# Optimization experiments

Hardware: AMD Instinct MI355X
Metric: run time of the kernel (lower is better)

Reference implementation:

```python
import jax, jax.numpy as jnp
import numpy as np

TAG_SIZE = 32
START = 30
STOP = 31
NEG = -10000.0
V, D, H, T = 100000, 256, 512, 4096  # vocab, embed_dim, hidden_dim, seq_len
HD = H // 2  # per-direction hidden


def setup_inputs() -> dict:
    key = jax.random.key(0)
    ks = jax.random.split(key, 12)
    s = 1.0 / np.sqrt(HD)

    def lstm_params(k):
        k1, k2, k3, k4 = jax.random.split(k, 4)
        return (jax.random.uniform(k1, (4 * HD, D), minval=-s, maxval=s),
                jax.random.uniform(k2, (4 * HD, HD), minval=-s, maxval=s),
                jax.random.uniform(k3, (4 * HD,), minval=-s, maxval=s),
                jax.random.uniform(k4, (4 * HD,), minval=-s, maxval=s))

    Wih_f, Whh_f, bih_f, bhh_f = lstm_params(ks[0])
    Wih_b, Whh_b, bih_b, bhh_b = lstm_params(ks[1])
    seq = jax.random.randint(ks[2], (T,), 0, V)
    E = jax.random.normal(ks[3], (V, D)) * 0.02
    h0 = jax.random.normal(ks[4], (2, HD))  # torch.randn initial hidden (fwd, bwd)
    c0 = jax.random.normal(ks[5], (2, HD))
    W_out = jax.random.normal(ks[6], (TAG_SIZE, H)) * 0.02
    b_out = jnp.zeros((TAG_SIZE,))
    transitions = jax.random.normal(ks[7], (TAG_SIZE, TAG_SIZE))
    transitions = transitions.at[START, :].set(NEG).at[:, STOP].set(NEG)
    return dict(seq=seq, E=E,
                Wih_f=Wih_f, Whh_f=Whh_f, bih_f=bih_f, bhh_f=bhh_f,
                Wih_b=Wih_b, Whh_b=Whh_b, bih_b=bih_b, bhh_b=bhh_b,
                h0=h0, c0=c0, W_out=W_out, b_out=b_out, transitions=transitions)


def _lstm_dir(x, h0, c0, Wih, Whh, bih, bhh):
    # x: (T, D). Precompute input projections for all steps at once.
    xg = x @ Wih.T + (bih + bhh)  # (T, 4*HD)

    def step(carry, xt):
        h, c = carry
        g = xt + h @ Whh.T
        i, f, gg, o = jnp.split(g, 4)  # torch gate order: i, f, g, o
        i = jax.nn.sigmoid(i); f = jax.nn.sigmoid(f)
        gg = jnp.tanh(gg); o = jax.nn.sigmoid(o)
        c = f * c + i * gg
        h = o * jnp.tanh(c)
        return (h, c), h

    _, hs = jax.lax.scan(step, (h0, c0), xg)
    return hs  # (T, HD)


def reference(seq, E, Wih_f, Whh_f, bih_f, bhh_f, Wih_b, Whh_b, bih_b, bhh_b,
              h0, c0, W_out, b_out, transitions):
    x = E[seq]  # (T, D)
    hf = _lstm_dir(x, h0[0], c0[0], Wih_f, Whh_f, bih_f, bhh_f)
    hb = _lstm_dir(x[::-1], h0[1], c0[1], Wih_b, Whh_b, bih_b, bhh_b)[::-1]
    feats = jnp.concatenate([hf, hb], axis=-1) @ W_out.T + b_out  # (T, TAG)

    # Viterbi: fused per-step (TAG x TAG) max-plus update in one scan.
    init = jnp.full((TAG_SIZE,), NEG).at[START].set(0.0)

    def vstep(fv, feat):
        scores = fv[None, :] + transitions  # [next_tag, prev_tag]
        bp = jnp.argmax(scores, axis=1)     # backpointers (emission is constant per next_tag)
        fv = jnp.max(scores, axis=1) + feat
        return fv, bp

    fv, bps = jax.lax.scan(vstep, init, feats)
    terminal = fv + transitions[STOP]
    best = jnp.argmax(terminal)
    score = terminal[best]

    def btstep(b, bp):
        nb = bp[b]
        return nb, nb

    _, path_rev = jax.lax.scan(btstep, best, bps[::-1])
    # drop the step into <START>, reverse, append terminal best tag -> length T
    path = jnp.concatenate([path_rev[::-1][1:], best[None]])
    return score, path
```

## Files before the change

### kernel.cpp

```cpp
#include <hip/hip_runtime.h>
#include <hip/hip_bf16.h>
#include <stdint.h>

#define T_LEN 4096
#define D_DIM 256
#define HDIM 256
#define G4 1024
#define NTAGS 32
#define START_TAG 30
#define STOP_TAG 31

typedef unsigned long long u64;
typedef unsigned int u32;

__device__ __forceinline__ float sigf(float x){ return 1.0f/(1.0f+expf(-x)); }

__global__ __launch_bounds__(256) void k_xg(const int* __restrict__ seq,
    const float* __restrict__ E,
    const float* __restrict__ Wf, const float* __restrict__ bihf, const float* __restrict__ bhhf,
    const float* __restrict__ Wb, const float* __restrict__ bihb, const float* __restrict__ bhhb,
    float* __restrict__ xg_f, float* __restrict__ xg_b)
{
    __shared__ __align__(16) float xsh[8][D_DIM];
    __shared__ int sq[8];
    const int b = blockIdx.x, tb = b >> 3, cb = b & 7, j = threadIdx.x;
    if (j < 8) sq[j] = seq[tb*8 + j];
    __syncthreads();
    #pragma unroll
    for (int r = 0; r < 8; ++r) xsh[r][j] = E[(size_t)sq[r]*D_DIM + j];
    __syncthreads();
    const int col = cb*256 + j;
    const int d   = col >> 10;
    const int row = col & 1023;
    const float* W = d ? Wb : Wf;
    const float bias = d ? (bihb[row] + bhhb[row]) : (bihf[row] + bhhf[row]);
    const float4* wr = reinterpret_cast<const float4*>(W + (size_t)row*D_DIM);
    float acc[8];
    #pragma unroll
    for (int r=0;r<8;++r) acc[r] = 0.f;
    for (int kk = 0; kk < D_DIM/4; ++kk){
        float4 wv = wr[kk];
        #pragma unroll
        for (int r=0;r<8;++r){
            float4 xv = reinterpret_cast<const float4*>(xsh[r])[kk];
            acc[r] = fmaf(wv.x, xv.x, fmaf(wv.y, xv.y, fmaf(wv.z, xv.z, fmaf(wv.w, xv.w, acc[r]))));
        }
    }
    #pragma unroll
    for (int r=0;r<8;++r){
        const int t = tb*8 + r;
        const float v = acc[r] + bias;
        if (d == 0) xg_f[(size_t)t*G4 + row] = v;
        else        xg_b[(size_t)(T_LEN-1-t)*G4 + row] = v;
    }
}

__global__ __launch_bounds__(256,1) void k_lstm(
    const float* __restrict__ Whh_f, const float* __restrict__ Whh_b,
    const float* __restrict__ xgf, const float* __restrict__ xgb,
    const float* __restrict__ h0, const float* __restrict__ c0,
    float* __restrict__ hs_f, float* __restrict__ hs_b,
    u64* __restrict__ hbuf_all)
{
    const int blk = blockIdx.x;
    const int d   = blk >> 5;
    const int sb  = blk & 31;
    const int ulo = sb * 8;
    const int j = threadIdx.x;
    const int r = j & 31;
    const int o = j >> 5;
    const int g_r = r >> 3;
    const int u_r = r & 7;
    const int row_global = g_r*256 + ulo + u_r;

    const float* __restrict__ Whh = d ? Whh_b : Whh_f;
    const float* __restrict__ xg  = d ? xgb : xgf;
    float* __restrict__ hs = d ? hs_b : hs_f;
    u64* __restrict__ hb = hbuf_all + (size_t)d*2*HDIM;

    __shared__ __align__(16) char wbuf[32*1024];
    __shared__ float h_sh[HDIM];
    __shared__ float partial[2*256];

    {
        const float4* src = reinterpret_cast<const float4*>(Whh + (size_t)row_global*HDIM + o*32);
        #pragma unroll
        for (int i = 0; i < 8; ++i){
            *reinterpret_cast<float4*>(wbuf + ((r*1024 + (o*8+i)*16) ^ ((r&7)<<4))) = src[i];
        }
    }
    h_sh[j] = h0[d*HDIM + j];
    float c = (j < 8) ? c0[d*HDIM + ulo + j] : 0.0f;
    float xgc = xg[row_global];
    __syncthreads();

    for (int t = 0; t < T_LEN; ++t){
        if (t > 0){
            const u32 want = (u32)t;
            u64* p = &hb[(size_t)(t&1)*HDIM + j];
            u64 pk = __hip_atomic_load(p, __ATOMIC_RELAXED, __HIP_MEMORY_SCOPE_AGENT);
            while ((u32)(pk >> 32) != want){
                pk = __hip_atomic_load(p, __ATOMIC_RELAXED, __HIP_MEMORY_SCOPE_AGENT);
            }
            h_sh[j] = __uint_as_float((u32)pk);
            asm volatile("s_waitcnt lgkmcnt(0)" ::: "memory");
        }
        float acc = 0.0f;
        {
            const float4* hvp = reinterpret_cast<const float4*>(h_sh + o*32);
            #pragma unroll
            for (int i = 0; i < 8; ++i){
                float4 wv = *reinterpret_cast<const float4*>(wbuf + ((r*1024 + (o*8+i)*16) ^ ((r&7)<<4)));
                float4 hv = hvp[i];
                acc = fmaf(wv.x, hv.x, fmaf(wv.y, hv.y, fmaf(wv.z, hv.z, fmaf(wv.w, hv.w, acc))));
            }
        }
        partial[(t&1)*256 + o*32 + r] = acc;
        __syncthreads();
        if (j < 32){
            const int par = t & 1;
            float s = xgc;
            #pragma unroll
            for (int oo = 0; oo < 8; ++oo) s += partial[par*256 + oo*32 + j];
            const float val = (g_r == 2) ? tanhf(s) : sigf(s);
            const float fv_ = __shfl(val,  8 + u_r, 64);
            const float gv_ = __shfl(val, 16 + u_r, 64);
            const float ov_ = __shfl(val, 24 + u_r, 64);
            if (j < 8){
                c = fv_*c + val*gv_;
                const float h = ov_*tanhf(c);
                const int ug = ulo + j;
                const u64 pk = ((u64)(u32)(t+1) << 32) | (u64)__float_as_uint(h);
                __hip_atomic_store(&hb[(size_t)((t+1)&1)*HDIM + ug], pk,
                                   __ATOMIC_RELAXED, __HIP_MEMORY_SCOPE_AGENT);
                hs[(size_t)(d==0 ? t : (T_LEN-1-t))*HDIM + ug] = h;
            }
            if (t+1 < T_LEN) xgc = xg[(size_t)(t+1)*G4 + row_global];
        }
    }
}

__global__ __launch_bounds__(256) void k_feats(
    const float* __restrict__ hs_f, const float* __restrict__ hs_b,
    const float* __restrict__ W_out, const float* __restrict__ b_out,
    float* __restrict__ feats)
{
    __shared__ __align__(16) float fsh[8][512];
    const int tb = blockIdx.x, j = threadIdx.x;
    #pragma unroll
    for (int r=0;r<8;++r){
        const int t = tb*8 + r;
        fsh[r][j]       = hs_f[(size_t)t*HDIM + j];
        fsh[r][256 + j] = hs_b[(size_t)t*HDIM + j];
    }
    __syncthreads();
    const int tsub = j >> 5, tag = j & 31;
    const float4* wr = reinterpret_cast<const float4*>(W_out + (size_t)tag*512);
    float acc = b_out[tag];
    for (int kk=0; kk<128; ++kk){
        float4 wvv = wr[kk];
        float4 hv = reinterpret_cast<const float4*>(fsh[tsub])[kk];
        acc = fmaf(wvv.x, hv.x, fmaf(wvv.y, hv.y, fmaf(wvv.z, hv.z, fmaf(wvv.w, hv.w, acc))));
    }
    feats[(size_t)(tb*8+tsub)*NTAGS + tag] = acc;
}

__global__ __launch_bounds__(256,1) void k_viterbi(
    const float* __restrict__ feats, const float* __restrict__ trans,
    unsigned char* __restrict__ bp_g, float* __restrict__ out)
{
    __shared__ __align__(16) float fbuf[2][256*NTAGS];
    __shared__ float fv_sh[NTAGS];
    __shared__ float term_sh[NTAGS];
    __shared__ int best_sh;
    const int j = threadIdx.x;
    const int n = j & 31, ph = (j >> 5) & 1;
    const bool scanlane = (j < 64);
    float tr[16];
    if (scanlane){
        #pragma unroll
        for (int i=0;i<16;++i) tr[i] = trans[n*NTAGS + ph*16 + i];
    }
    float fv = (n == START_TAG) ? 0.0f : -10000.0f;

    const int CH = 256, NCH = T_LEN / CH;
    for (int idx = j; idx < CH*NTAGS; idx += 256) fbuf[0][idx] = feats[idx];
    __syncthreads();
    for (int cc = 0; cc < NCH; ++cc){
        const int buf = cc & 1;
        if (scanlane){
            for (int s = 0; s < CH; ++s){
                const int t = cc*CH + s;
                const float f = fbuf[buf][s*NTAGS + n];
                if (ph == 0) fv_sh[n] = fv;
                float bestv = -1e30f; int bestp = 0;
                #pragma unroll
                for (int i=0;i<16;++i){
                    const int p = ph*16 + i;
                    const float v = fv_sh[p] + tr[i];
                    if (v > bestv){ bestv = v; bestp = p; }
                }
                const float ov = __shfl_xor(bestv, 32, 64);
                const int   op = __shfl_xor(bestp, 32, 64);
                const float lowv  = ph ? ov    : bestv;
                const int   lowp  = ph ? op    : bestp;
                const float highv = ph ? bestv : ov;
                const int   highp = ph ? bestp : op;
                float wvv = lowv; int wp = lowp;
                if (highv > lowv){ wvv = highv; wp = highp; }
                if (ph == 0) bp_g[(size_t)t*NTAGS + n] = (unsigned char)wp;
                fv = wvv + f;
            }
        } else if (cc + 1 < NCH){
            const int nb = (cc+1) & 1;
            const float* src = feats + (size_t)(cc+1)*CH*NTAGS;
            for (int idx = j - 64; idx < CH*NTAGS; idx += 192) fbuf[nb][idx] = src[idx];
        }
        __syncthreads();
    }

    if (scanlane && ph == 0) term_sh[n] = fv + trans[STOP_TAG*NTAGS + n];
    __syncthreads();
    if (j == 0){
        float bv = term_sh[0]; int bi = 0;
        for (int p = 1; p < NTAGS; ++p){
            if (term_sh[p] > bv){ bv = term_sh[p]; bi = p; }
        }
        out[0] = bv;
        out[1 + (T_LEN-1)] = (float)bi;
        best_sh = bi;
    }
    __syncthreads();
    unsigned char* bp_sh = reinterpret_cast<unsigned char*>(fbuf);
    int b = best_sh;
    for (int cc2 = 3; cc2 >= 0; --cc2){
        const u32* src = reinterpret_cast<const u32*>(bp_g + (size_t)cc2*1024*NTAGS);
        u32* dst = reinterpret_cast<u32*>(bp_sh);
        for (int idx = j; idx < 8192; idx += 256) dst[idx] = src[idx];
        __syncthreads();
        if (j == 0){
            for (int tt = 1023; tt >= 0; --tt){
                const int t = cc2*1024 + tt;
                if (t == 0) break;
                const int nb2 = bp_sh[tt*NTAGS + b];
                out[1 + (t-1)] = (float)nb2;
                b = nb2;
            }
        }
        __syncthreads();
    }
}

extern "C" void kernel_launch(void* const* d_in, const int* in_sizes, int n_in,
                              void* d_out, int out_size, void* d_ws, size_t ws_size,
                              hipStream_t stream)
{
    const int*   seq   = (const int*)  d_in[0];
    const float* E     = (const float*)d_in[1];
    const float* Wih_f = (const float*)d_in[2];
    const float* Whh_f = (const float*)d_in[3];
    const float* bih_f = (const float*)d_in[4];
    const float* bhh_f = (const float*)d_in[5];
    const float* Wih_b = (const float*)d_in[6];
    const float* Whh_b = (const float*)d_in[7];
    const float* bih_b = (const float*)d_in[8];
    const float* bhh_b = (const float*)d_in[9];
    const float* h0    = (const float*)d_in[10];
    const float* c0    = (const float*)d_in[11];
    const float* W_out = (const float*)d_in[12];
    const float* b_out = (const float*)d_in[13];
    const float* trans = (const float*)d_in[14];

    char* ws = (char*)d_ws;
    float* xg_f  = (float*)(ws);
    float* xg_b  = (float*)(ws + (size_t)(16u<<20));
    float* hs_f  = (float*)(ws + (size_t)(32u<<20));
    float* hs_b  = (float*)(ws + (size_t)(36u<<20));
    float* feats = (float*)(ws + (size_t)(40u<<20));
    unsigned char* bp = (unsigned char*)(ws + (size_t)(40u<<20) + (512u<<10));
    u64* hbuf    = (u64*)(ws + (size_t)(40u<<20) + (640u<<10));

    k_xg<<<dim3(4096), dim3(256), 0, stream>>>(seq, E, Wih_f, bih_f, bhh_f,
                                               Wih_b, bih_b, bhh_b, xg_f, xg_b);
    k_lstm<<<dim3(64), dim3(256), 0, stream>>>(Whh_f, Whh_b, xg_f, xg_b, h0, c0, hs_f, hs_b, hbuf);
    k_feats<<<dim3(512), dim3(256), 0, stream>>>(hs_f, hs_b, W_out, b_out, feats);
    k_viterbi<<<dim3(1), dim3(256), 0, stream>>>(feats, trans, bp, (float*)d_out);
}
```

Baseline: 6.950 ms.

## Shrink LSTM recurrence to 8 blocks per direction with 128KB LDS weights

The persistent LSTM kernel now runs 8 workgroups per direction instead of 32. Each workgroup owns 32 hidden units (128 gate rows, 128KB of Whh in LDS), and each row is split across two lanes that are reduced with a shuffle rather than a shared-memory partial-sum pass. Locally produced h values are written straight into a double-buffered shared array, so only the other 224 units are polled from global memory each step. The aim is fewer participants in the cross-block spin synchronisation and less intra-block reduction latency per timestep. The cost is more serial FMA work per thread (128 FMAs) and very large LDS use per block.

```diff
diff --git a/kernel.cpp b/kernel.cpp
--- a/kernel.cpp
+++ b/kernel.cpp
@@ -63,80 +63,87 @@
     u64* __restrict__ hbuf_all)
 {
     const int blk = blockIdx.x;
-    const int d   = blk >> 5;
-    const int sb  = blk & 31;
-    const int ulo = sb * 8;
+    const int d   = blk >> 3;
+    const int sb  = blk & 7;
+    const int ulo = sb * 32;
     const int j = threadIdx.x;
-    const int r = j & 31;
-    const int o = j >> 5;
-    const int g_r = r >> 3;
-    const int u_r = r & 7;
-    const int row_global = g_r*256 + ulo + u_r;
+    const int w = j >> 6;
+    const int l = j & 63;
+    const int half = l & 1;
+    const int rb   = w*32 + (l >> 1);
+    const int g_r  = rb & 3;
+    const int u_loc= rb >> 2;
+    const int row_global = g_r*256 + ulo + u_loc;
+    const bool prod = ((l & 7) == 0);
+    const int ug = ulo + w*8 + (l >> 3);
 
     const float* __restrict__ Whh = d ? Whh_b : Whh_f;
     const float* __restrict__ xg  = d ? xgb : xgf;
     float* __restrict__ hs = d ? hs_b : hs_f;
     u64* __restrict__ hb = hbuf_all + (size_t)d*2*HDIM;
 
-    __shared__ __align__(16) char wbuf[32*1024];
-    __shared__ float h_sh[HDIM];
-    __shared__ float partial[2*256];
+    __shared__ __align__(16) char wbuf[128*1024];
+    __shared__ float h_sh[2][HDIM];
 
     {
-        const float4* src = reinterpret_cast<const float4*>(Whh + (size_t)row_global*HDIM + o*32);
+        const float4* src = reinterpret_cast<const float4*>(Whh + (size_t)row_global*HDIM + half*128);
         #pragma unroll
-        for (int i = 0; i < 8; ++i){
-            *reinterpret_cast<float4*>(wbuf + ((r*1024 + (o*8+i)*16) ^ ((r&7)<<4))) = src[i];
-        }
-    }
-    h_sh[j] = h0[d*HDIM + j];
-    float c = (j < 8) ? c0[d*HDIM + ulo + j] : 0.0f;
-    float xgc = xg[row_global];
+        for (int i = 0; i < 32; ++i){
+            const int byte = (rb*1024 + half*512 + i*16) ^ ((rb&7)<<4);
+            *reinterpret_cast<float4*>(wbuf + byte) = src[i];
+        }
+    }
+    h_sh[0][j] = h0[d*HDIM + j];
+    float c = 0.0f;
+    if (prod) c = c0[d*HDIM + ug];
+    float xgc = (half == 0) ? xg[row_global] : 0.0f;
     __syncthreads();
 
     for (int t = 0; t < T_LEN; ++t){
+        const int par = t & 1;
         if (t > 0){
-            const u32 want = (u32)t;
-            u64* p = &hb[(size_t)(t&1)*HDIM + j];
-            u64 pk = __hip_atomic_load(p, __ATOMIC_RELAXED, __HIP_MEMORY_SCOPE_AGENT);
-            while ((u32)(pk >> 32) != want){
-                pk = __hip_atomic_load(p, __ATOMIC_RELAXED, __HIP_MEMORY_SCOPE_AGENT);
-            }
-            h_sh[j] = __uint_as_float((u32)pk);
-            asm volatile("s_waitcnt lgkmcnt(0)" ::: "memory");
-        }
+            const bool own = (j >= ulo) && (j < ulo + 32);
+            if (!own){
+                const u32 want = (u32)t;
+                u64* p = &hb[(size_t)par*HDIM + j];
+                u64 pk = __hip_atomic_load(p, __ATOMIC_RELAXED, __HIP_MEMORY_SCOPE_AGENT);
+                while ((u32)(pk >> 32) != want){
+                    pk = __hip_atomic_load(p, __ATOMIC_RELAXED, __HIP_MEMORY_SCOPE_AGENT);
+                }
+                h_sh[par][j] = __uint_as_float((u32)pk);
+            }
+        }
+        __syncthreads();
+
         float acc = 0.0f;
         {
-            const float4* hvp = reinterpret_cast<const float4*>(h_sh + o*32);
+            const float* hbase = h_sh[par] + half*128;
             #pragma unroll
-            for (int i = 0; i < 8; ++i){
-                float4 wv = *reinterpret_cast<const float4*>(wbuf + ((r*1024 + (o*8+i)*16) ^ ((r&7)<<4)));
-                float4 hv = hvp[i];
+            for (int i = 0; i < 32; ++i){
+                const int byte = (rb*1024 + half*512 + i*16) ^ ((rb&7)<<4);
+                const float4 wv = *reinterpret_cast<const float4*>(wbuf + byte);
+                const float4 hv = *reinterpret_cast<const float4*>(hbase + i*4);
                 acc = fmaf(wv.x, hv.x, fmaf(wv.y, hv.y, fmaf(wv.z, hv.z, fmaf(wv.w, hv.w, acc))));
             }
         }
-        partial[(t&1)*256 + o*32 + r] = acc;
-        __syncthreads();
-        if (j < 32){
-            const int par = t & 1;
-            float s = xgc;
-            #pragma unroll
-            for (int oo = 0; oo < 8; ++oo) s += partial[par*256 + oo*32 + j];
-            const float val = (g_r == 2) ? tanhf(s) : sigf(s);
-            const float fv_ = __shfl(val,  8 + u_r, 64);
-            const float gv_ = __shfl(val, 16 + u_r, 64);
-            const float ov_ = __shfl(val, 24 + u_r, 64);
-            if (j < 8){
-                c = fv_*c + val*gv_;
-                const float h = ov_*tanhf(c);
-                const int ug = ulo + j;
-                const u64 pk = ((u64)(u32)(t+1) << 32) | (u64)__float_as_uint(h);
-                __hip_atomic_store(&hb[(size_t)((t+1)&1)*HDIM + ug], pk,
-                                   __ATOMIC_RELAXED, __HIP_MEMORY_SCOPE_AGENT);
-                hs[(size_t)(d==0 ? t : (T_LEN-1-t))*HDIM + ug] = h;
-            }
-            if (t+1 < T_LEN) xgc = xg[(size_t)(t+1)*G4 + row_global];
-        }
+        const float other = __shfl_xor(acc, 1, 64);
+        const float sfull = (half == 0) ? (xgc + (acc + other)) : 0.0f;
+        const float val = (g_r == 2) ? tanhf(sfull) : sigf(sfull);
+        const int base = l & 56;
+        const float f_ = __shfl(val, base + 2, 64);
+        const float g_ = __shfl(val, base + 4, 64);
+        const float o_ = __shfl(val, base + 6, 64);
+        if (prod){
+            c = f_*c + val*g_;
+            const float h = o_*tanhf(c);
+            const u64 pk = ((u64)(u32)(t+1) << 32) | (u64)__float_as_uint(h);
+            __hip_atomic_store(&hb[(size_t)((t+1)&1)*HDIM + ug], pk,
+                               __ATOMIC_RELAXED, __HIP_MEMORY_SCOPE_AGENT);
+            h_sh[(t+1)&1][ug] = h;
+            hs[(size_t)(d==0 ? t : (T_LEN-1-t))*HDIM + ug] = h;
+        }
+        if (half == 0 && t+1 < T_LEN)
+            xgc = xg[(size_t)(t+1)*G4 + row_global];
     }
 }
 
@@ -282,7 +289,7 @@
 
     k_xg<<<dim3(4096), dim3(256), 0, stream>>>(seq, E, Wih_f, bih_f, bhh_f,
                                                Wih_b, bih_b, bhh_b, xg_f, xg_b);
-    k_lstm<<<dim3(64), dim3(256), 0, stream>>>(Whh_f, Whh_b, xg_f, xg_b, h0, c0, hs_f, hs_b, hbuf);
+    k_lstm<<<dim3(16), dim3(256), 0, stream>>>(Whh_f, Whh_b, xg_f, xg_b, h0, c0, hs_f, hs_b, hbuf);
     k_feats<<<dim3(512), dim3(256), 0, stream>>>(hs_f, hs_b, W_out, b_out, feats);
     k_viterbi<<<dim3(1), dim3(256), 0, stream>>>(feats, trans, bp, (float*)d_out);
 }
```

After: 9.937 ms. 43.0% more time.

## Retile input projection to 128 timesteps per block and split LSTM gate reduction across waves

Applied to the files above, without the earlier changes.

The input-projection kernel now handles 128 timesteps per block, in four chunks of 32 rows each, so every weight row loaded from global memory is reused across 32 timesteps instead of 8, and the grid shrinks from 4096 to 256 blocks. In the recurrent LSTM kernel, partial dot products are first combined within each wave with a cross-lane shuffle. The gate nonlinearities and cell update are then spread over four waves, two hidden units each, instead of running serially in a single 32-lane group. The goal is to shorten the per-step critical path of the sequential recurrence and to cut redundant weight traffic in the projection. In exchange, the projection kernel holds 32 accumulators per thread and gets far fewer blocks, which may reduce occupancy and latency hiding.

```diff
diff --git a/kernel.cpp b/kernel.cpp
--- a/kernel.cpp
+++ b/kernel.cpp
@@ -21,37 +21,43 @@
     const float* __restrict__ Wb, const float* __restrict__ bihb, const float* __restrict__ bhhb,
     float* __restrict__ xg_f, float* __restrict__ xg_b)
 {
-    __shared__ __align__(16) float xsh[8][D_DIM];
-    __shared__ int sq[8];
-    const int b = blockIdx.x, tb = b >> 3, cb = b & 7, j = threadIdx.x;
-    if (j < 8) sq[j] = seq[tb*8 + j];
-    __syncthreads();
-    #pragma unroll
-    for (int r = 0; r < 8; ++r) xsh[r][j] = E[(size_t)sq[r]*D_DIM + j];
-    __syncthreads();
+    __shared__ __align__(16) float xsh[32][D_DIM];
+    const int cb = blockIdx.x & 7;
+    const int tg = blockIdx.x >> 3;
+    const int j  = threadIdx.x;
     const int col = cb*256 + j;
     const int d   = col >> 10;
     const int row = col & 1023;
     const float* W = d ? Wb : Wf;
     const float bias = d ? (bihb[row] + bhhb[row]) : (bihf[row] + bhhf[row]);
     const float4* wr = reinterpret_cast<const float4*>(W + (size_t)row*D_DIM);
-    float acc[8];
-    #pragma unroll
-    for (int r=0;r<8;++r) acc[r] = 0.f;
-    for (int kk = 0; kk < D_DIM/4; ++kk){
-        float4 wv = wr[kk];
+
+    for (int s = 0; s < 4; ++s){
+        const int t0 = tg*128 + s*32;
+        __syncthreads();
+        for (int r2 = 0; r2 < 32; ++r2){
+            const int sqv = seq[t0 + r2];
+            xsh[r2][j] = E[(size_t)sqv*D_DIM + j];
+        }
+        __syncthreads();
+        float acc[32];
         #pragma unroll
-        for (int r=0;r<8;++r){
-            float4 xv = reinterpret_cast<const float4*>(xsh[r])[kk];
-            acc[r] = fmaf(wv.x, xv.x, fmaf(wv.y, xv.y, fmaf(wv.z, xv.z, fmaf(wv.w, xv.w, acc[r]))));
-        }
-    }
-    #pragma unroll
-    for (int r=0;r<8;++r){
-        const int t = tb*8 + r;
-        const float v = acc[r] + bias;
-        if (d == 0) xg_f[(size_t)t*G4 + row] = v;
-        else        xg_b[(size_t)(T_LEN-1-t)*G4 + row] = v;
+        for (int r2 = 0; r2 < 32; ++r2) acc[r2] = 0.f;
+        for (int kk = 0; kk < D_DIM/4; ++kk){
+            const float4 wv = wr[kk];
+            #pragma unroll
+            for (int r2 = 0; r2 < 32; ++r2){
+                const float4 xv = reinterpret_cast<const float4*>(xsh[r2])[kk];
+                acc[r2] = fmaf(wv.x, xv.x, fmaf(wv.y, xv.y, fmaf(wv.z, xv.z, fmaf(wv.w, xv.w, acc[r2]))));
+            }
+        }
+        #pragma unroll
+        for (int r2 = 0; r2 < 32; ++r2){
+            const int t = t0 + r2;
+            const float v = acc[r2] + bias;
+            if (d == 0) xg_f[(size_t)t*G4 + row] = v;
+            else        xg_b[(size_t)(T_LEN-1-t)*G4 + row] = v;
+        }
     }
 }
 
@@ -69,6 +75,8 @@
     const int j = threadIdx.x;
     const int r = j & 31;
     const int o = j >> 5;
+    const int w = j >> 6;
+    const int l = j & 63;
     const int g_r = r >> 3;
     const int u_r = r & 7;
     const int row_global = g_r*256 + ulo + u_r;
@@ -80,7 +88,7 @@
 
     __shared__ __align__(16) char wbuf[32*1024];
     __shared__ float h_sh[HDIM];
-    __shared__ float partial[2*256];
+    __shared__ float partial[2*128];
 
     {
         const float4* src = reinterpret_cast<const float4*>(Whh + (size_t)row_global*HDIM + o*32);
@@ -90,18 +98,22 @@
         }
     }
     h_sh[j] = h0[d*HDIM + j];
-    float c = (j < 8) ? c0[d*HDIM + ulo + j] : 0.0f;
-    float xgc = xg[row_global];
+
+    const int g2 = l >> 1;
+    const int u2 = 2*w + (l & 1);
+    const int gate_row_global = g2*256 + ulo + u2;
+    float c   = (l < 2) ? c0[d*HDIM + ulo + u2] : 0.0f;
+    float xgc = (l < 8) ? xg[gate_row_global] : 0.0f;
     __syncthreads();
 
     for (int t = 0; t < T_LEN; ++t){
+        const int par = t & 1;
         if (t > 0){
             const u32 want = (u32)t;
-            u64* p = &hb[(size_t)(t&1)*HDIM + j];
+            u64* p = &hb[(size_t)par*HDIM + j];
             u64 pk = __hip_atomic_load(p, __ATOMIC_RELAXED, __HIP_MEMORY_SCOPE_AGENT);
-            while ((u32)(pk >> 32) != want){
+            while ((u32)(pk >> 32) != want)
                 pk = __hip_atomic_load(p, __ATOMIC_RELAXED, __HIP_MEMORY_SCOPE_AGENT);
-            }
             h_sh[j] = __uint_as_float((u32)pk);
             asm volatile("s_waitcnt lgkmcnt(0)" ::: "memory");
         }
@@ -115,27 +127,28 @@
                 acc = fmaf(wv.x, hv.x, fmaf(wv.y, hv.y, fmaf(wv.z, hv.z, fmaf(wv.w, hv.w, acc))));
             }
         }
-        partial[(t&1)*256 + o*32 + r] = acc;
-        __syncthreads();
-        if (j < 32){
-            const int par = t & 1;
-            float s = xgc;
-            #pragma unroll
-            for (int oo = 0; oo < 8; ++oo) s += partial[par*256 + oo*32 + j];
-            const float val = (g_r == 2) ? tanhf(s) : sigf(s);
-            const float fv_ = __shfl(val,  8 + u_r, 64);
-            const float gv_ = __shfl(val, 16 + u_r, 64);
-            const float ov_ = __shfl(val, 24 + u_r, 64);
-            if (j < 8){
-                c = fv_*c + val*gv_;
-                const float h = ov_*tanhf(c);
-                const int ug = ulo + j;
+        acc += __shfl_xor(acc, 32, 64);
+        if ((j & 32) == 0) partial[par*128 + w*32 + r] = acc;
+        __syncthreads();
+        if (l < 8){
+            const int rr = g2*8 + u2;
+            const float* pp = partial + par*128;
+            const float s = xgc + ((pp[rr] + pp[32+rr]) + (pp[64+rr] + pp[96+rr]));
+            const float val = (g2 == 2) ? tanhf(s) : sigf(s);
+            const float f_ = __shfl(val, 2 + (l&1), 64);
+            const float g_ = __shfl(val, 4 + (l&1), 64);
+            const float o_ = __shfl(val, 6 + (l&1), 64);
+            if (l < 2){
+                c = f_*c + val*g_;
+                const float h = o_*tanhf(c);
+                const int ug = ulo + u2;
                 const u64 pk = ((u64)(u32)(t+1) << 32) | (u64)__float_as_uint(h);
                 __hip_atomic_store(&hb[(size_t)((t+1)&1)*HDIM + ug], pk,
                                    __ATOMIC_RELAXED, __HIP_MEMORY_SCOPE_AGENT);
                 hs[(size_t)(d==0 ? t : (T_LEN-1-t))*HDIM + ug] = h;
             }
-            if (t+1 < T_LEN) xgc = xg[(size_t)(t+1)*G4 + row_global];
+            if (t+1 < T_LEN)
+                xgc = xg[(size_t)(t+1)*G4 + gate_row_global];
         }
     }
 }
@@ -280,8 +293,8 @@
     unsigned char* bp = (unsigned char*)(ws + (size_t)(40u<<20) + (512u<<10));
     u64* hbuf    = (u64*)(ws + (size_t)(40u<<20) + (640u<<10));
 
-    k_xg<<<dim3(4096), dim3(256), 0, stream>>>(seq, E, Wih_f, bih_f, bhh_f,
-                                               Wih_b, bih_b, bhh_b, xg_f, xg_b);
+    k_xg<<<dim3(256), dim3(256), 0, stream>>>(seq, E, Wih_f, bih_f, bhh_f,
+                                              Wih_b, bih_b, bhh_b, xg_f, xg_b);
     k_lstm<<<dim3(64), dim3(256), 0, stream>>>(Whh_f, Whh_b, xg_f, xg_b, h0, c0, hs_f, hs_b, hbuf);
     k_feats<<<dim3(512), dim3(256), 0, stream>>>(hs_f, hs_b, W_out, b_out, feats);
     k_viterbi<<<dim3(1), dim3(256), 0, stream>>>(feats, trans, bp, (float*)d_out);
```

Measured after the change: 9.292 ms. 33.7% more time.

## Parallelize Viterbi forward pass via chunked max-plus transfer matrices

Applied to the files above, without the earlier changes.

Replaces the single-block sequential Viterbi scan with a chunked max-plus scan. One kernel computes a 32x32 transfer matrix for each 64-step chunk, a second propagates seeds across chunks, a third recomputes backpointers per chunk in parallel, and a fourth does the final backtrace. This removes the serial dependency over 4096 steps and replaces it with parallel chunk work and a 64-step serial combine. The cost is three extra launches and redundant work, and tie-breaking in argmax could diverge through different float summation order.

```diff
diff --git a/kernel.cpp b/kernel.cpp
--- a/kernel.cpp
+++ b/kernel.cpp
@@ -95,13 +95,13 @@
     __syncthreads();
 
     for (int t = 0; t < T_LEN; ++t){
+        const int par = t & 1;
         if (t > 0){
             const u32 want = (u32)t;
-            u64* p = &hb[(size_t)(t&1)*HDIM + j];
+            u64* p = &hb[(size_t)par*HDIM + j];
             u64 pk = __hip_atomic_load(p, __ATOMIC_RELAXED, __HIP_MEMORY_SCOPE_AGENT);
-            while ((u32)(pk >> 32) != want){
+            while ((u32)(pk >> 32) != want)
                 pk = __hip_atomic_load(p, __ATOMIC_RELAXED, __HIP_MEMORY_SCOPE_AGENT);
-            }
             h_sh[j] = __uint_as_float((u32)pk);
             asm volatile("s_waitcnt lgkmcnt(0)" ::: "memory");
         }
@@ -115,20 +115,19 @@
                 acc = fmaf(wv.x, hv.x, fmaf(wv.y, hv.y, fmaf(wv.z, hv.z, fmaf(wv.w, hv.w, acc))));
             }
         }
-        partial[(t&1)*256 + o*32 + r] = acc;
+        partial[par*256 + o*32 + r] = acc;
         __syncthreads();
         if (j < 32){
-            const int par = t & 1;
             float s = xgc;
             #pragma unroll
             for (int oo = 0; oo < 8; ++oo) s += partial[par*256 + oo*32 + j];
             const float val = (g_r == 2) ? tanhf(s) : sigf(s);
-            const float fv_ = __shfl(val,  8 + u_r, 64);
-            const float gv_ = __shfl(val, 16 + u_r, 64);
-            const float ov_ = __shfl(val, 24 + u_r, 64);
+            const float f_ = __shfl(val,  8 + u_r, 64);
+            const float g_ = __shfl(val, 16 + u_r, 64);
+            const float o_ = __shfl(val, 24 + u_r, 64);
             if (j < 8){
-                c = fv_*c + val*gv_;
-                const float h = ov_*tanhf(c);
+                c = f_*c + val*g_;
+                const float h = o_*tanhf(c);
                 const int ug = ulo + j;
                 const u64 pk = ((u64)(u32)(t+1) << 32) | (u64)__float_as_uint(h);
                 __hip_atomic_store(&hb[(size_t)((t+1)&1)*HDIM + ug], pk,
@@ -165,61 +164,116 @@
     feats[(size_t)(tb*8+tsub)*NTAGS + tag] = acc;
 }
 
-__global__ __launch_bounds__(256,1) void k_viterbi(
+__global__ __launch_bounds__(256,1) void k_vitA(
     const float* __restrict__ feats, const float* __restrict__ trans,
-    unsigned char* __restrict__ bp_g, float* __restrict__ out)
-{
-    __shared__ __align__(16) float fbuf[2][256*NTAGS];
+    float* __restrict__ G)
+{
+    const int chunk = blockIdx.x >> 3;
+    const int sg    = blockIdx.x & 7;
+    const int w = threadIdx.x >> 6;
+    const int l = threadIdx.x & 63;
+    const int q = sg*4 + w;
+    const int n = l & 31, ph = (l >> 5) & 1;
+    __shared__ float fv_sh[4][NTAGS];
+    float tr[16];
+    #pragma unroll
+    for (int i=0;i<16;++i) tr[i] = trans[n*NTAGS + ph*16 + i];
+    float fv = (n == q) ? 0.0f : -1e9f;
+    const int t0 = chunk*64;
+    for (int s = 0; s < 64; ++s){
+        const float f = feats[(size_t)(t0+s)*NTAGS + n];
+        if (ph == 0) fv_sh[w][n] = fv;
+        float bestv = -1e30f;
+        #pragma unroll
+        for (int i=0;i<16;++i){
+            const float v = fv_sh[w][ph*16 + i] + tr[i];
+            if (v > bestv) bestv = v;
+        }
+        const float ov = __shfl_xor(bestv, 32, 64);
+        fv = fmaxf(bestv, ov) + f;
+    }
+    if (ph == 0) G[((size_t)chunk*NTAGS + n)*NTAGS + q] = fv;
+}
+
+__global__ __launch_bounds__(256,1) void k_vitB(
+    const float* __restrict__ G, float* __restrict__ seeds)
+{
+    __shared__ float Gs[NTAGS*33];
+    __shared__ float s_sh[NTAGS];
+    const int j = threadIdx.x;
+    if (j < NTAGS){
+        const float s0 = (j == START_TAG) ? 0.0f : -10000.0f;
+        s_sh[j] = s0;
+        seeds[j] = s0;
+    }
+    __syncthreads();
+    for (int c = 0; c < 64; ++c){
+        for (int idx = j; idx < NTAGS*NTAGS; idx += 256)
+            Gs[(idx >> 5)*33 + (idx & 31)] = G[(size_t)c*NTAGS*NTAGS + idx];
+        __syncthreads();
+        float nv = 0.0f;
+        if (j < NTAGS){
+            float b = -1e30f;
+            #pragma unroll
+            for (int qq = 0; qq < NTAGS; ++qq)
+                b = fmaxf(b, Gs[j*33 + qq] + s_sh[qq]);
+            nv = b;
+        }
+        __syncthreads();
+        if (j < NTAGS){
+            s_sh[j] = nv;
+            seeds[(size_t)(c+1)*NTAGS + j] = nv;
+        }
+        __syncthreads();
+    }
+}
+
+__global__ __launch_bounds__(64,1) void k_vitC(
+    const float* __restrict__ feats, const float* __restrict__ trans,
+    const float* __restrict__ seeds, unsigned char* __restrict__ bp_g)
+{
+    const int chunk = blockIdx.x;
+    const int l = threadIdx.x;
+    const int n = l & 31, ph = (l >> 5) & 1;
     __shared__ float fv_sh[NTAGS];
+    float tr[16];
+    #pragma unroll
+    for (int i=0;i<16;++i) tr[i] = trans[n*NTAGS + ph*16 + i];
+    float fv = seeds[(size_t)chunk*NTAGS + n];
+    const int t0 = chunk*64;
+    for (int s = 0; s < 64; ++s){
+        const int t = t0 + s;
+        const float f = feats[(size_t)t*NTAGS + n];
+        if (ph == 0) fv_sh[n] = fv;
+        float bestv = -1e30f; int bestp = 0;
+        #pragma unroll
+        for (int i=0;i<16;++i){
+            const int p = ph*16 + i;
+            const float v = fv_sh[p] + tr[i];
+            if (v > bestv){ bestv = v; bestp = p; }
+        }
+        const float ov = __shfl_xor(bestv, 32, 64);
+        const int   op = __shfl_xor(bestp, 32, 64);
+        const float lowv  = ph ? ov    : bestv;
+        const int   lowp  = ph ? op    : bestp;
+        const float highv = ph ? bestv : ov;
+        const int   highp = ph ? bestp : op;
+        float wvv = lowv; int wp = lowp;
+        if (highv > lowv){ wvv = highv; wp = highp; }
+        if (ph == 0) bp_g[(size_t)t*NTAGS + n] = (unsigned char)wp;
+        fv = wvv + f;
+    }
+}
+
+__global__ __launch_bounds__(256,1) void k_vitD(
+    const float* __restrict__ seeds, const float* __restrict__ trans,
+    const unsigned char* __restrict__ bp_g, float* __restrict__ out)
+{
+    __shared__ __align__(16) char bp_sh[32*1024];
     __shared__ float term_sh[NTAGS];
     __shared__ int best_sh;
     const int j = threadIdx.x;
-    const int n = j & 31, ph = (j >> 5) & 1;
-    const bool scanlane = (j < 64);
-    float tr[16];
-    if (scanlane){
-        #pragma unroll
-        for (int i=0;i<16;++i) tr[i] = trans[n*NTAGS + ph*16 + i];
-    }
-    float fv = (n == START_TAG) ? 0.0f : -10000.0f;
-
-    const int CH = 256, NCH = T_LEN / CH;
-    for (int idx = j; idx < CH*NTAGS; idx += 256) fbuf[0][idx] = feats[idx];
-    __syncthreads();
-    for (int cc = 0; cc < NCH; ++cc){
-        const int buf = cc & 1;
-        if (scanlane){
-            for (int s = 0; s < CH; ++s){
-                const int t = cc*CH + s;
-                const float f = fbuf[buf][s*NTAGS + n];
-                if (ph == 0) fv_sh[n] = fv;
-                float bestv = -1e30f; int bestp = 0;
-                #pragma unroll
-                for (int i=0;i<16;++i){
-                    const int p = ph*16 + i;
-                    const float v = fv_sh[p] + tr[i];
-                    if (v > bestv){ bestv = v; bestp = p; }
-                }
-                const float ov = __shfl_xor(bestv, 32, 64);
-                const int   op = __shfl_xor(bestp, 32, 64);
-                const float lowv  = ph ? ov    : bestv;
-                const int   lowp  = ph ? op    : bestp;
-                const float highv = ph ? bestv : ov;
-                const int   highp = ph ? bestp : op;
-                float wvv = lowv; int wp = lowp;
-                if (highv > lowv){ wvv = highv; wp = highp; }
-                if (ph == 0) bp_g[(size_t)t*NTAGS + n] = (unsigned char)wp;
-                fv = wvv + f;
-            }
-        } else if (cc + 1 < NCH){
-            const int nb = (cc+1) & 1;
-            const float* src = feats + (size_t)(cc+1)*CH*NTAGS;
-            for (int idx = j - 64; idx < CH*NTAGS; idx += 192) fbuf[nb][idx] = src[idx];
-        }
-        __syncthreads();
-    }
-
-    if (scanlane && ph == 0) term_sh[n] = fv + trans[STOP_TAG*NTAGS + n];
+    if (j < NTAGS) term_sh[j] = seeds[(size_t)64*NTAGS + j] + trans[STOP_TAG*NTAGS + j];
     __syncthreads();
     if (j == 0){
         float bv = term_sh[0]; int bi = 0;
@@ -231,7 +285,6 @@
         best_sh = bi;
     }
     __syncthreads();
-    unsigned char* bp_sh = reinterpret_cast<unsigned char*>(fbuf);
     int b = best_sh;
     for (int cc2 = 3; cc2 >= 0; --cc2){
         const u32* src = reinterpret_cast<const u32*>(bp_g + (size_t)cc2*1024*NTAGS);
@@ -279,10 +332,15 @@
     float* feats = (float*)(ws + (size_t)(40u<<20));
     unsigned char* bp = (unsigned char*)(ws + (size_t)(40u<<20) + (512u<<10));
     u64* hbuf    = (u64*)(ws + (size_t)(40u<<20) + (640u<<10));
+    float* Gmat  = (float*)(ws + (size_t)(41u<<20));
+    float* seeds = (float*)(ws + (size_t)(41u<<20) + (256u<<10));
 
     k_xg<<<dim3(4096), dim3(256), 0, stream>>>(seq, E, Wih_f, bih_f, bhh_f,
                                                Wih_b, bih_b, bhh_b, xg_f, xg_b);
     k_lstm<<<dim3(64), dim3(256), 0, stream>>>(Whh_f, Whh_b, xg_f, xg_b, h0, c0, hs_f, hs_b, hbuf);
     k_feats<<<dim3(512), dim3(256), 0, stream>>>(hs_f, hs_b, W_out, b_out, feats);
-    k_viterbi<<<dim3(1), dim3(256), 0, stream>>>(feats, trans, bp, (float*)d_out);
-}
+    k_vitA<<<dim3(512), dim3(256), 0, stream>>>(feats, trans, Gmat);
+    k_vitB<<<dim3(1),   dim3(256), 0, stream>>>(Gmat, seeds);
+    k_vitC<<<dim3(64),  dim3(64),  0, stream>>>(feats, trans, seeds, bp);
+    k_vitD<<<dim3(1),   dim3(256), 0, stream>>>(seeds, trans, bp, (float*)d_out);
+}
```

Result: faster. 6.132 ms, median of 2 (-11.8%).
